# Kernel optimization log

Hardware: AMD Instinct MI355X
Metric: run time of the kernel (lower is better)

## Reference

```python
import jax, jax.numpy as jnp
import numpy as np

VOCAB = 100000
DIM = 512
BLOCK_LEN = 4
NUM_BLOCKS = DIM // BLOCK_LEN          # 128
NUM_CODES = 256                        # 2**bits_per_block, bits_per_block = 8
BATCH, SEQ = 32, 4096


def setup_inputs() -> dict:
    key = jax.random.key(0)
    k1, k2, k3 = jax.random.split(key, 3)
    # Token/row indices into the compressed embedding table (forward arg `input`).
    input_ids = jax.random.randint(k1, (BATCH, SEQ), 0, VOCAB, dtype=jnp.int32)
    # Dense equivalent of the bit-packed bin_rep: per-row, per-block codebook indices.
    codes = jax.random.randint(k2, (VOCAB, NUM_BLOCKS), 0, NUM_CODES, dtype=jnp.int32)
    # Codebook centroids: [2**bits_per_block, block_len].
    codebook = jax.random.normal(k3, (NUM_CODES, BLOCK_LEN), dtype=jnp.float32)
    return {"input_ids": input_ids, "codes": codes, "codebook": codebook}


def reference(input_ids, codes, codebook):
    # Smallfry.decode: for each queried row, unpack its num_blocks codebook ids
    # and concatenate the corresponding centroids into a dim-length embedding.
    row_codes = codes[input_ids]                 # [B, S, NUM_BLOCKS] int
    blocks = codebook[row_codes]                 # [B, S, NUM_BLOCKS, BLOCK_LEN]
    return blocks.reshape(input_ids.shape + (DIM,))  # [B, S, DIM]
```

## Files before the change

kernel.cpp:

```cpp
#include <hip/hip_runtime.h>


#define NUM_BLOCKS 128
#define NUM_CODES  256
#define NTOK       (32 * 4096)

__global__ __launch_bounds__(256) void smallfry_decode_kernel(
    const int* __restrict__ input_ids,
    const int* __restrict__ codes,
    const float4* __restrict__ codebook,
    float4* __restrict__ out)
{
    __shared__ float4 cb[NUM_CODES];
    if (threadIdx.x < NUM_CODES) {
        cb[threadIdx.x] = codebook[threadIdx.x];
    }
    __syncthreads();

    const int gtid   = blockIdx.x * blockDim.x + threadIdx.x;
    const int lane   = gtid & 63;
    const int wave   = gtid >> 6;
    const int nwaves = (gridDim.x * blockDim.x) >> 6;

    for (int token = wave; token < NTOK; token += nwaves) {
        const int row = input_ids[token];
        const int2* crow = reinterpret_cast<const int2*>(codes + (long long)row * NUM_BLOCKS);
        const int2 cc = crow[lane];

        const float4 v0 = cb[cc.x];
        const float4 v1 = cb[cc.y];

        float4* orow = out + (long long)token * (NUM_BLOCKS) + lane * 2;
        orow[0] = v0;
        orow[1] = v1;
    }
}

extern "C" void kernel_launch(void* const* d_in, const int* in_sizes, int n_in,
                              void* d_out, int out_size, void* d_ws, size_t ws_size,
                              hipStream_t stream) {
    const int*    input_ids = (const int*)d_in[0];
    const int*    codes     = (const int*)d_in[1];
    const float4* codebook  = (const float4*)d_in[2];
    float4*       out       = (float4*)d_out;

    const int block = 256;
    const int grid  = 4096;
    smallfry_decode_kernel<<<grid, block, 0, stream>>>(input_ids, codes, codebook, out);
}
```

Measured before the change: 332.3 us.

## Batch 16 tokens per wave with shuffled ids and nontemporal coalesced stores

Measured after the change: 307.8 us. 1.08x faster.

```diff
diff --git a/kernel.cpp b/kernel.cpp
--- a/kernel.cpp
+++ b/kernel.cpp
@@ -4,47 +4,56 @@
 #define NUM_BLOCKS 128
 #define NUM_CODES  256
 #define NTOK       (32 * 4096)
+#define TOK_PER_WAVE 16
 
-__global__ __launch_bounds__(256) void smallfry_decode_kernel(
+typedef float f32x4 __attribute__((ext_vector_type(4)));
+
+__global__ __launch_bounds__(256, 8) void smallfry_decode_kernel(
     const int* __restrict__ input_ids,
     const int* __restrict__ codes,
-    const float4* __restrict__ codebook,
-    float4* __restrict__ out)
+    const f32x4* __restrict__ codebook,
+    f32x4* __restrict__ out)
 {
-    __shared__ float4 cb[NUM_CODES];
+    __shared__ f32x4 cb[NUM_CODES];
     if (threadIdx.x < NUM_CODES) {
         cb[threadIdx.x] = codebook[threadIdx.x];
     }
     __syncthreads();
 
-    const int gtid   = blockIdx.x * blockDim.x + threadIdx.x;
-    const int lane   = gtid & 63;
-    const int wave   = gtid >> 6;
-    const int nwaves = (gridDim.x * blockDim.x) >> 6;
+    const int gtid = blockIdx.x * blockDim.x + threadIdx.x;
+    const int lane = gtid & 63;
+    const int wave = gtid >> 6;
 
-    for (int token = wave; token < NTOK; token += nwaves) {
-        const int row = input_ids[token];
-        const int2* crow = reinterpret_cast<const int2*>(codes + (long long)row * NUM_BLOCKS);
-        const int2 cc = crow[lane];
+    const int base = wave * TOK_PER_WAVE;
 
-        const float4 v0 = cb[cc.x];
-        const float4 v1 = cb[cc.y];
+    int tok_id = 0;
+    if (lane < TOK_PER_WAVE) tok_id = input_ids[base + lane];
 
-        float4* orow = out + (long long)token * (NUM_BLOCKS) + lane * 2;
-        orow[0] = v0;
-        orow[1] = v1;
+#pragma unroll 4
+    for (int t = 0; t < TOK_PER_WAVE; ++t) {
+        const int row = __shfl(tok_id, t);
+        const int* crow = codes + (long long)row * NUM_BLOCKS;
+        const int c0 = crow[lane];
+        const int c1 = crow[lane + 64];
+
+        const f32x4 v0 = cb[c0];
+        const f32x4 v1 = cb[c1];
+
+        f32x4* orow = out + (size_t)(base + t) * NUM_BLOCKS;
+        __builtin_nontemporal_store(v0, &orow[lane]);
+        __builtin_nontemporal_store(v1, &orow[lane + 64]);
     }
 }
 
 extern "C" void kernel_launch(void* const* d_in, const int* in_sizes, int n_in,
                               void* d_out, int out_size, void* d_ws, size_t ws_size,
                               hipStream_t stream) {
-    const int*    input_ids = (const int*)d_in[0];
-    const int*    codes     = (const int*)d_in[1];
-    const float4* codebook  = (const float4*)d_in[2];
-    float4*       out       = (float4*)d_out;
+    const int*   input_ids = (const int*)d_in[0];
+    const int*   codes     = (const int*)d_in[1];
+    const f32x4* codebook  = (const f32x4*)d_in[2];
+    f32x4*       out       = (f32x4*)d_out;
 
     const int block = 256;
-    const int grid  = 4096;
+    const int grid  = (NTOK / TOK_PER_WAVE) / 4;
     smallfry_decode_kernel<<<grid, block, 0, stream>>>(input_ids, codes, codebook, out);
 }
```
